# Kernel optimization log

Hardware: AMD Instinct MI355X
Metric: run time of the kernel (lower is better)

Reference implementation:

```python
import jax, jax.numpy as jnp
import numpy as np

NUM_CLASS = 22  # restypes_with_x_and_gap


def setup_inputs() -> dict:
    key = jax.random.key(0)
    k1, k2, k3, k4 = jax.random.split(key, 4)
    b, m, n, c = 1, 128, 256, NUM_CLASS
    variant = jax.random.randint(k1, (b, m, n), 0, c)              # int variant sequences
    variant_mask = jnp.ones((b, m, n), dtype=jnp.float32)
    eij = jax.random.normal(k2, (b, n, n, c, c), dtype=jnp.float32) * 0.1  # Potts couplings wij
    ei = jax.random.normal(k3, (b, n, c), dtype=jnp.float32) * 0.1         # fields bi
    mask_vec = jnp.ones((c,), dtype=jnp.float32).at[-1].set(0.0)   # mask out gap '-' class
    sigma = jnp.ones((1,), dtype=jnp.float32)                      # prior_w=1.0, task_num=1
    return {"variant": variant, "variant_mask": variant_mask, "eij": eij,
            "ei": ei, "mask_vec": mask_vec, "sigma": sigma}


def reference(variant, variant_mask, eij, ei, mask_vec, sigma):
    c = mask_vec.shape[0]
    onehot = jax.nn.one_hot(variant, c, dtype=eij.dtype)           # [b,m,n,c]
    # fold class mask into couplings, then Potts energy per position/class
    em = eij * mask_vec                                            # [b,i,j,c,d]
    hi = jnp.einsum('bmjd,bijcd->bmic', onehot, em)                # [b,m,i,c]
    motifs = ei[:, None] + hi                                      # [b,m,i,c]
    # log_softmax=False branch: pick the logit of the active class per position
    logits = jnp.einsum('bmic,bmic->bmi', motifs, onehot)          # [b,m,i]
    # eval path: delta vs reference variant (index 0), sum-pooled, scaled by sigma
    vm = variant_mask[..., None]                                   # [b,m,i,1]
    vm = vm * vm[:, :1]
    vlogit = logits - logits[:, :1]                                # [b,m,i]
    pooled = jnp.sum(vlogit[..., None] * vm, axis=-2)              # [b,m,task_num]
    variant_logit = sigma * pooled
    return motifs, logits, variant_logit
```

## Files before the change

kernel.cpp:

```cpp
#include <hip/hip_runtime.h>

#define NC    22
#define NI    256
#define NJ    256
#define NM    128
#define JG    8
#define NSS   (NJ/JG)
#define SLOT  512
#define MOTLD 23

typedef __attribute__((ext_vector_type(8))) short short8;
typedef __attribute__((ext_vector_type(4))) float f32x4;

__device__ __forceinline__ uint32_t bf16rne(float x) {
    uint32_t u = __float_as_uint(x);
    u += 0x7FFFu + ((u >> 16) & 1u);
    return u >> 16;
}

__device__ __forceinline__ uint32_t pk_bf16(float lo, float hi) {
    uint32_t r;
    asm("v_cvt_pk_bf16_f32 %0, %1, %2" : "=v"(r) : "v"(lo), "v"(hi));
    return r;
}

__device__ __forceinline__ void gload_lds16(const void* g, void* l) {
    __builtin_amdgcn_global_load_lds(
        (const __attribute__((address_space(1))) void*)g,
        (__attribute__((address_space(3))) void*)l, 16, 0, 0);
}

union u32x4s8 { uint32_t u[4]; short8 s; };

__global__ __launch_bounds__(1024) void potts_fused(
    const int*   __restrict__ variant,
    const float* __restrict__ eij,
    const float* __restrict__ ei,
    const float* __restrict__ mask_vec,
    float*       __restrict__ out_motifs,
    float*       __restrict__ out_logits)
{
    const int i    = blockIdx.x;
    const int tid  = threadIdx.x;
    const int lane = tid & 63;
    const int w    = tid >> 6;
    const int jl   = w >> 1;
    const int mh   = w & 1;
    const int q    = lane >> 4;
    const int nl   = lane & 15;
    const int c1   = 16 + nl;

    __shared__ float    tile[2][JG][SLOT];
    __shared__ int      vtab[2][NM * JG];
    __shared__ uint32_t maskTab[32];

    if (tid < 32) maskTab[tid] = (tid < NC) ? bf16rne(mask_vec[tid]) : 0u;
    if (tid < 2 * JG * (SLOT - 484)) {
        const int b = tid / (JG * 28), r = tid % (JG * 28);
        tile[b][r / 28][484 + (r % 28)] = 0.f;
    }

    const int    poff  = mh ? 228 : 0;
    const size_t ebase = ((size_t)i * NJ + jl) * 484 + poff + lane * 4;
    const bool vstage = (w >= 8) && ((w & 1) == 0);
    const int  pidx   = (w - 8) >> 1;
    const int  vmrow  = (pidx * 32 + (lane >> 1)) * NJ + (lane & 1) * 4;

    gload_lds16(eij + ebase, &tile[0][jl][poff]);
    if (vstage) gload_lds16(variant + vmrow, &vtab[0][pidx * 256]);

    f32x4 acc[4][2];
    #pragma unroll
    for (int mt = 0; mt < 4; ++mt) {
        acc[mt][0] = (f32x4){0.f, 0.f, 0.f, 0.f};
        acc[mt][1] = (f32x4){0.f, 0.f, 0.f, 0.f};
    }

    for (int s = 0; s < NSS; ++s) {
        const int cur = s & 1;
        __syncthreads();
        if (s + 1 < NSS) {
            const int nxt = cur ^ 1;
            gload_lds16(eij + ebase + (size_t)(s + 1) * (JG * 484),
                        &tile[nxt][jl][poff]);
            if (vstage)
                gload_lds16(variant + vmrow + (s + 1) * JG,
                            &vtab[nxt][pidx * 256]);
        }

        const float* jrow = &tile[cur][jl][0];
        const float* r0 = jrow + nl * NC + q * 8;
        const float* r1 = jrow + (c1 < NC ? c1 : 0) * NC + q * 8;
        const float2 x0 = *(const float2*)(r0 + 0);
        const float2 x1 = *(const float2*)(r0 + 2);
        const float2 x2 = *(const float2*)(r0 + 4);
        const float2 x3 = *(const float2*)(r0 + 6);
        const float2 y0 = *(const float2*)(r1 + 0);
        const float2 y1 = *(const float2*)(r1 + 2);
        const float2 y2 = *(const float2*)(r1 + 4);
        const float2 y3 = *(const float2*)(r1 + 6);
        u32x4s8 B0, B1;
        B0.u[0] = pk_bf16(x0.x, x0.y);  B0.u[1] = pk_bf16(x1.x, x1.y);
        B0.u[2] = pk_bf16(x2.x, x2.y);  B0.u[3] = pk_bf16(x3.x, x3.y);
        B1.u[0] = pk_bf16(y0.x, y0.y);  B1.u[1] = pk_bf16(y1.x, y1.y);
        B1.u[2] = pk_bf16(y2.x, y2.y);  B1.u[3] = pk_bf16(y3.x, y3.y);

        const int* vt = vtab[cur];
        const int  kb = q * 4;
        #pragma unroll
        for (int mt = 0; mt < 4; ++mt) {
            const int      va = vt[(mh * 64 + mt * 16 + nl) * JG + jl] & 31;
            const uint32_t pa = maskTab[va] << ((va & 1) << 4);
            const int      ha = va >> 1;
            u32x4s8 A;
            #pragma unroll
            for (int t = 0; t < 4; ++t) A.u[t] = (ha == kb + t) ? pa : 0u;
            acc[mt][0] = __builtin_amdgcn_mfma_f32_16x16x32_bf16(A.s, B0.s, acc[mt][0], 0, 0, 0);
            acc[mt][1] = __builtin_amdgcn_mfma_f32_16x16x32_bf16(A.s, B1.s, acc[mt][1], 0, 0, 0);
        }
    }

    __syncthreads();
    float* mot = &tile[0][0][0];
    for (int p = tid; p < NM * MOTLD; p += 1024) mot[p] = 0.f;
    __syncthreads();
    #pragma unroll
    for (int mt = 0; mt < 4; ++mt) {
        #pragma unroll
        for (int t = 0; t < 4; ++t) {
            const int row = mh * 64 + mt * 16 + q * 4 + t;
            atomicAdd(&mot[row * MOTLD + nl], acc[mt][0][t]);
            if (c1 < NC) atomicAdd(&mot[row * MOTLD + c1], acc[mt][1][t]);
        }
    }
    __syncthreads();
    const float* eirow = ei + i * NC;
    for (int p = tid; p < NM * 32; p += 1024) {
        const int m = p >> 5, c = p & 31;
        if (c < NC)
            out_motifs[((size_t)m * NI + i) * NC + c] = mot[m * MOTLD + c] + eirow[c];
    }
    if (tid < NM) {
        const int vi = variant[tid * NJ + i];
        out_logits[tid * NI + i] = mot[tid * MOTLD + vi] + eirow[vi];
    }
}

__global__ __launch_bounds__(64) void potts_pool(
    const float* __restrict__ logits,
    const float* __restrict__ vmask,
    const float* __restrict__ sigma,
    float*       __restrict__ out_vl)
{
    const int m    = blockIdx.x;
    const int lane = threadIdx.x;
    float s = 0.f;
    #pragma unroll
    for (int qq = 0; qq < 4; ++qq) {
        const int i = lane + 64 * qq;
        const float vl = logits[m * NI + i] - logits[i];
        s += vl * vmask[m * NI + i] * vmask[i];
    }
    #pragma unroll
    for (int off = 32; off > 0; off >>= 1)
        s += __shfl_down(s, off, 64);
    if (lane == 0) out_vl[m] = sigma[0] * s;
}

extern "C" void kernel_launch(void* const* d_in, const int* in_sizes, int n_in,
                              void* d_out, int out_size, void* d_ws, size_t ws_size,
                              hipStream_t stream) {
    const int*   variant  = (const int*)  d_in[0];
    const float* vmask    = (const float*)d_in[1];
    const float* eij      = (const float*)d_in[2];
    const float* ei       = (const float*)d_in[3];
    const float* mask_vec = (const float*)d_in[4];
    const float* sigma    = (const float*)d_in[5];

    float* out        = (float*)d_out;
    float* out_motifs = out;
    float* out_logits = out_motifs + NM * NI * NC;
    float* out_vl     = out_logits + NM * NI;

    potts_fused<<<NI, 1024, 0, stream>>>(variant, eij, ei, mask_vec,
                                         out_motifs, out_logits);
    potts_pool<<<NM, 64, 0, stream>>>(out_logits, vmask, sigma, out_vl);
}
```

Measured before the change: 234.2 us.

## Deepen eij LDS pipeline to four stages and preload variant table as bytes

The eij staging ring grows from two to four LDS buffers with three tiles in flight. Explicit vmcnt waits plus a raw s_barrier replace the per-step __syncthreads, aiming to hide global-load latency behind the MFMA work. The whole variant matrix is loaded once into a transposed byte table in LDS, which removes per-step variant streaming. The mask pattern shift is also precomputed into a table. The trade-off is more LDS per block and a serial upfront variant load, and correctness now depends on vmcnt accounting and the single barrier per step guarding reuse of the ring slots.

Result: slower. 251.5 us (+7.4%).

```diff
diff --git a/kernel.cpp b/kernel.cpp
--- a/kernel.cpp
+++ b/kernel.cpp
@@ -7,6 +7,7 @@
 #define JG    8
 #define NSS   (NJ/JG)
 #define SLOT  512
+#define DEPTH 4
 #define MOTLD 23
 
 typedef __attribute__((ext_vector_type(8))) short short8;
@@ -30,6 +31,8 @@
         (__attribute__((address_space(3))) void*)l, 16, 0, 0);
 }
 
+#define WAITV(n) asm volatile("s_waitcnt vmcnt(" #n ")" ::: "memory")
+
 union u32x4s8 { uint32_t u[4]; short8 s; };
 
 __global__ __launch_bounds__(1024) void potts_fused(
@@ -49,25 +52,31 @@
     const int q    = lane >> 4;
     const int nl   = lane & 15;
     const int c1   = 16 + nl;
+    const int c1r  = (c1 < NC) ? c1 : 0;
+    const int kb   = q * 4;
 
-    __shared__ float    tile[2][JG][SLOT];
-    __shared__ int      vtab[2][NM * JG];
-    __shared__ uint32_t maskTab[32];
+    __shared__ float         tile[DEPTH][JG][SLOT];
+    __shared__ unsigned char vt8[NJ][NM];
+    __shared__ uint32_t      patTab[32];
 
-    if (tid < 32) maskTab[tid] = (tid < NC) ? bf16rne(mask_vec[tid]) : 0u;
-    if (tid < 2 * JG * (SLOT - 484)) {
-        const int b = tid / (JG * 28), r = tid % (JG * 28);
+    if (tid < 32) {
+        const uint32_t mb = (tid < NC) ? bf16rne(mask_vec[tid]) : 0u;
+        patTab[tid] = mb << ((tid & 1) << 4);
+    }
+    for (int p = tid; p < DEPTH * JG * (SLOT - 484); p += 1024) {
+        const int b = p / (JG * 28), r = p % (JG * 28);
         tile[b][r / 28][484 + (r % 28)] = 0.f;
     }
+    for (int p = tid; p < NM * NJ; p += 1024)
+        vt8[p & (NJ - 1)][p >> 8] = (unsigned char)variant[p];
+    __syncthreads();
 
     const int    poff  = mh ? 228 : 0;
     const size_t ebase = ((size_t)i * NJ + jl) * 484 + poff + lane * 4;
-    const bool vstage = (w >= 8) && ((w & 1) == 0);
-    const int  pidx   = (w - 8) >> 1;
-    const int  vmrow  = (pidx * 32 + (lane >> 1)) * NJ + (lane & 1) * 4;
 
-    gload_lds16(eij + ebase, &tile[0][jl][poff]);
-    if (vstage) gload_lds16(variant + vmrow, &vtab[0][pidx * 256]);
+    gload_lds16(eij + ebase,                           &tile[0][jl][poff]);
+    gload_lds16(eij + ebase + (size_t)1 * (JG * 484),  &tile[1][jl][poff]);
+    gload_lds16(eij + ebase + (size_t)2 * (JG * 484),  &tile[2][jl][poff]);
 
     f32x4 acc[4][2];
     #pragma unroll
@@ -77,20 +86,19 @@
     }
 
     for (int s = 0; s < NSS; ++s) {
-        const int cur = s & 1;
-        __syncthreads();
-        if (s + 1 < NSS) {
-            const int nxt = cur ^ 1;
-            gload_lds16(eij + ebase + (size_t)(s + 1) * (JG * 484),
-                        &tile[nxt][jl][poff]);
-            if (vstage)
-                gload_lds16(variant + vmrow + (s + 1) * JG,
-                            &vtab[nxt][pidx * 256]);
-        }
+        if      (s <= NSS - 3) WAITV(2);
+        else if (s == NSS - 2) WAITV(1);
+        else                   WAITV(0);
+        __builtin_amdgcn_s_barrier();
+        asm volatile("" ::: "memory");
 
-        const float* jrow = &tile[cur][jl][0];
+        if (s + 3 < NSS)
+            gload_lds16(eij + ebase + (size_t)(s + 3) * (JG * 484),
+                        &tile[(s + 3) & 3][jl][poff]);
+
+        const float* jrow = &tile[s & 3][jl][0];
         const float* r0 = jrow + nl * NC + q * 8;
-        const float* r1 = jrow + (c1 < NC ? c1 : 0) * NC + q * 8;
+        const float* r1 = jrow + c1r * NC + q * 8;
         const float2 x0 = *(const float2*)(r0 + 0);
         const float2 x1 = *(const float2*)(r0 + 2);
         const float2 x2 = *(const float2*)(r0 + 4);
@@ -105,12 +113,11 @@
         B1.u[0] = pk_bf16(y0.x, y0.y);  B1.u[1] = pk_bf16(y1.x, y1.y);
         B1.u[2] = pk_bf16(y2.x, y2.y);  B1.u[3] = pk_bf16(y3.x, y3.y);
 
-        const int* vt = vtab[cur];
-        const int  kb = q * 4;
+        const unsigned char* vrow = &vt8[s * JG + jl][mh * 64 + nl];
         #pragma unroll
         for (int mt = 0; mt < 4; ++mt) {
-            const int      va = vt[(mh * 64 + mt * 16 + nl) * JG + jl] & 31;
-            const uint32_t pa = maskTab[va] << ((va & 1) << 4);
+            const int      va = vrow[mt * 16];
+            const uint32_t pa = patTab[va];
             const int      ha = va >> 1;
             u32x4s8 A;
             #pragma unroll
@@ -141,7 +148,7 @@
             out_motifs[((size_t)m * NI + i) * NC + c] = mot[m * MOTLD + c] + eirow[c];
     }
     if (tid < NM) {
-        const int vi = variant[tid * NJ + i];
+        const int vi = vt8[i][tid];
         out_logits[tid * NI + i] = mot[tid * MOTLD + vi] + eirow[vi];
     }
 }
```
